# Kernel optimization log

Hardware: AMD Instinct MI355X
Metric: run time of the kernel (lower is better)

Reference implementation:

```python
import jax, jax.numpy as jnp
import numpy as np

D_MODEL = 1024
N_HEADS = 16
D_K = D_MODEL // N_HEADS  # 64


def setup_inputs() -> dict:
    key = jax.random.key(0)
    ks = jax.random.split(key, 12)
    B, S = 2, 2048
    inp = {
        "query": jax.random.normal(ks[0], (B, S, D_MODEL), jnp.float32),
        "key": jax.random.normal(ks[1], (B, S, D_MODEL), jnp.float32),
        "value": jax.random.normal(ks[2], (B, S, D_MODEL), jnp.float32),
        "mask": jnp.ones((B, 1, S, S), jnp.int32),
    }
    sc = 1.0 / np.sqrt(D_MODEL)
    inp["Wq"] = jax.random.normal(ks[3], (D_MODEL, D_MODEL), jnp.float32) * sc
    inp["bq"] = jnp.zeros((D_MODEL,), jnp.float32)
    inp["Wk"] = jax.random.normal(ks[4], (D_MODEL, D_MODEL), jnp.float32) * sc
    inp["bk"] = jnp.zeros((D_MODEL,), jnp.float32)
    inp["Wv"] = jax.random.normal(ks[5], (D_MODEL, D_MODEL), jnp.float32) * sc
    inp["bv"] = jnp.zeros((D_MODEL,), jnp.float32)
    inp["Wo"] = jax.random.normal(ks[6], (D_MODEL, D_MODEL), jnp.float32) * sc
    inp["bo"] = jnp.zeros((D_MODEL,), jnp.float32)
    return inp


def reference(query, key, value, mask, Wq, bq, Wk, bk, Wv, bv, Wo, bo):
    B, Sq, _ = query.shape
    H, dk = N_HEADS, D_K
    # linear projections, split heads: (B,S,D) -> (B,H,S,dk)
    def split_heads(x):
        return x.reshape(B, -1, H, dk).transpose(0, 2, 1, 3)
    Q = split_heads(query @ Wq.T + bq)
    K = split_heads(key @ Wk.T + bk)
    V = split_heads(value @ Wv.T + bv)
    scale = 1.0 / jnp.sqrt(jnp.asarray(dk, jnp.float32))
    scores = jnp.einsum('bhqd,bhkd->bhqk', Q, K) * scale
    scores = jnp.where(mask == 0, jnp.asarray(-1e9, scores.dtype), scores)
    attn = jax.nn.softmax(scores, axis=-1)  # (B,H,Sq,Sk)
    out = jnp.einsum('bhqk,bhkd->bhqd', attn, V)
    out = out.transpose(0, 2, 1, 3).reshape(B, Sq, D_MODEL)
    out = out @ Wo.T + bo
    return out, attn
```

## Files before the change

kernel.cpp:

```cpp
#include <hip/hip_runtime.h>
#include <cstdint>
#include <cstddef>

#define DEV __device__ __forceinline__

#define LGKM_BARRIER() asm volatile("s_waitcnt lgkmcnt(0)\n\ts_barrier" ::: "memory")

typedef float f32x4 __attribute__((ext_vector_type(4)));
typedef __bf16 bf16x8 __attribute__((ext_vector_type(8)));
typedef unsigned short u16x8 __attribute__((ext_vector_type(8)));

static constexpr int D = 1024, H = 16, DK = 64, S = 2048, B = 2;
static constexpr int M_TOT = B * S;
static constexpr size_t OUT0 = (size_t)M_TOT * D;

DEV unsigned short f2bf(float f) {
  unsigned x = __builtin_bit_cast(unsigned, f);
  unsigned r = (x + 0x7fffu + ((x >> 16) & 1u)) >> 16;
  return (unsigned short)r;
}

DEV float bf2f(unsigned short u) {
  return __builtin_bit_cast(float, (unsigned)u << 16);
}

DEV f32x4 mfma_bf16(bf16x8 a, bf16x8 b, f32x4 c) {
  return __builtin_amdgcn_mfma_f32_16x16x32_bf16(a, b, c, 0, 0, 0);
}

DEV bf16x8 bc(u16x8 u) { return __builtin_bit_cast(bf16x8, u); }

template <int MODE>
DEV void proj_body(unsigned short* As, unsigned short* Bs,
                   const unsigned short* A, const unsigned short* W,
                   const float* bias, void* dst) {
  constexpr int BM = 128, BK = 32, LDT = 40;
  const int tid = threadIdx.x;
  const int lane = tid & 63, wave = tid >> 6;
  const int wrow = wave >> 1, wcol = wave & 1;
  const int l15 = lane & 15, kg = lane >> 4;
  const int m0 = blockIdx.y * BM, n0 = blockIdx.x * BM;
  const int srow = tid >> 1, scb = (tid & 1) * 16;

  f32x4 acc[4][4] = {};

  for (int kt = 0; kt < D; kt += BK) {
    {
      const unsigned short* ap = A + (size_t)(m0 + srow) * D + kt + scb;
      *(u16x8*)&As[srow * LDT + scb] = *(const u16x8*)ap;
      *(u16x8*)&As[srow * LDT + scb + 8] = *(const u16x8*)(ap + 8);

      const unsigned short* wp = W + (size_t)(n0 + srow) * D + kt + scb;
      *(u16x8*)&Bs[srow * LDT + scb] = *(const u16x8*)wp;
      *(u16x8*)&Bs[srow * LDT + scb + 8] = *(const u16x8*)(wp + 8);
    }
    __syncthreads();

    bf16x8 a[4], b[4];
#pragma unroll
    for (int i = 0; i < 4; i++)
      a[i] = bc(*(const u16x8*)&As[(wrow * 64 + i * 16 + l15) * LDT + kg * 8]);
#pragma unroll
    for (int i = 0; i < 4; i++)
      b[i] = bc(*(const u16x8*)&Bs[(wcol * 64 + i * 16 + l15) * LDT + kg * 8]);
#pragma unroll
    for (int mi = 0; mi < 4; mi++)
#pragma unroll
      for (int ni = 0; ni < 4; ni++) acc[mi][ni] = mfma_bf16(a[mi], b[ni], acc[mi][ni]);
    __syncthreads();
  }

#pragma unroll
  for (int mi = 0; mi < 4; mi++) {
#pragma unroll
    for (int ni = 0; ni < 4; ni++) {
      const int n = n0 + wcol * 64 + ni * 16 + l15;
      const float bval = bias[n];
#pragma unroll
      for (int r = 0; r < 4; r++) {
        const int m = m0 + wrow * 64 + mi * 16 + kg * 4 + r;
        float v = acc[mi][ni][r] + bval;
        if constexpr (MODE == 0) v *= 0.125f;
        if constexpr (MODE == 0 || MODE == 1) {
          const int b_ = m >> 11, s = m & (S - 1), h = n >> 6, d_ = n & (DK - 1);
          ((unsigned short*)dst)[(((size_t)(b_ * H + h)) * S + s) * DK + d_] = f2bf(v);
        } else if constexpr (MODE == 2) {
          const int b_ = m >> 11, s = m & (S - 1), h = n >> 6, d_ = n & (DK - 1);
          ((unsigned short*)dst)[(((size_t)(b_ * H + h)) * DK + d_) * S + s] = f2bf(v);
        } else {
          ((float*)dst)[(size_t)m * D + n] = v;
        }
      }
    }
  }
}

struct ConvArgs {
  const float* src[7];
  unsigned short* dst[7];
  const int* mask;
  unsigned long long* bits;
};

__global__ __launch_bounds__(256) void conv_kernel(ConvArgs ca) {
  const int gid = blockIdx.x, tid = threadIdx.x;
  if (gid < 1024) {
    int seg, local;
    if (gid < 256) { seg = gid >> 6; local = gid & 63; }
    else { seg = 4 + ((gid - 256) >> 8); local = (gid - 256) & 255; }
    const float* src = ca.src[seg];
    unsigned short* dst = ca.dst[seg];
    const size_t off = (size_t)local * 16384;
#pragma unroll
    for (int it = 0; it < 4; it++) {
      const size_t i0 = off + it * 4096 + (size_t)tid * 16;
      float4 v0 = *(const float4*)(src + i0);
      float4 v1 = *(const float4*)(src + i0 + 4);
      float4 v2 = *(const float4*)(src + i0 + 8);
      float4 v3 = *(const float4*)(src + i0 + 12);
      u16x8 t0, t1;
      t0[0] = f2bf(v0.x); t0[1] = f2bf(v0.y); t0[2] = f2bf(v0.z); t0[3] = f2bf(v0.w);
      t0[4] = f2bf(v1.x); t0[5] = f2bf(v1.y); t0[6] = f2bf(v1.z); t0[7] = f2bf(v1.w);
      t1[0] = f2bf(v2.x); t1[1] = f2bf(v2.y); t1[2] = f2bf(v2.z); t1[3] = f2bf(v2.w);
      t1[4] = f2bf(v3.x); t1[5] = f2bf(v3.y); t1[6] = f2bf(v3.z); t1[7] = f2bf(v3.w);
      *(u16x8*)(dst + i0) = t0;
      *(u16x8*)(dst + i0 + 8) = t1;
    }
  } else {
    const int lane = tid & 63;
    const int base = (gid - 1024) * 256;
    for (int w = base + (tid >> 6); w < base + 256; w += 4) {
      int m = __builtin_nontemporal_load(ca.mask + (size_t)w * 64 + lane);
      unsigned long long bal = __ballot(m != 0);
      if (lane == 0) ca.bits[w] = bal;
    }
  }
}

struct GemmArgs {
  const unsigned short* Ab[3];
  const unsigned short* Wb[3];
  const float* bias[3];
  unsigned short* dst[3];
};

__global__ __launch_bounds__(256) void qkv_gemm(GemmArgs ga) {
  __shared__ __align__(16) unsigned short As[128 * 40];
  __shared__ __align__(16) unsigned short Bs[128 * 40];
  const int z = blockIdx.z;
  if (z == 0)
    proj_body<0>(As, Bs, ga.Ab[0], ga.Wb[0], ga.bias[0], ga.dst[0]);
  else if (z == 1)
    proj_body<1>(As, Bs, ga.Ab[1], ga.Wb[1], ga.bias[1], ga.dst[1]);
  else
    proj_body<2>(As, Bs, ga.Ab[2], ga.Wb[2], ga.bias[2], ga.dst[2]);
}

__global__ __launch_bounds__(256) void out_proj(const unsigned short* __restrict__ ctx,
                                                const unsigned short* __restrict__ Wob,
                                                const float* __restrict__ bo,
                                                float* __restrict__ out) {
  __shared__ __align__(16) unsigned short As[128 * 40];
  __shared__ __align__(16) unsigned short Bs[128 * 40];
  proj_body<3>(As, Bs, ctx, Wob, bo, out);
}

__global__ __launch_bounds__(512, 4) void attn_kernel(
    const unsigned short* __restrict__ Qb, const unsigned short* __restrict__ Kb,
    const unsigned short* __restrict__ Vt, const unsigned* __restrict__ bits32,
    float* __restrict__ attn_out, unsigned short* __restrict__ ctx) {
  constexpr int QB = 32;
  constexpr int PROW = 264;
  __shared__ __align__(16) unsigned short pbuf[2][QB * PROW];
  __shared__ float rsum[8 * QB];
  __shared__ float rinv_s[QB];
  __shared__ unsigned mflag;

  const int wg = blockIdx.x;
  const int qblk = wg & 63, h = (wg >> 6) & 15, b_ = wg >> 10;
  const int bh = b_ * H + h;
  const int qb0 = qblk * QB;
  const int tid = threadIdx.x, lane = tid & 63, wave = tid >> 6;
  const int l15 = lane & 15, kg = lane >> 4;
  const int rowq = kg * 4;
  constexpr float LOG2E = 1.44269504088896340736f;

  const unsigned* mrow = bits32 + ((size_t)b_ * S + qb0) * 64;

  if (tid == 0) mflag = 1u;
  __syncthreads();
  {
    unsigned ok = 1u;
#pragma unroll
    for (int i = 0; i < 4; i++)
      ok &= (mrow[tid + i * 512] == 0xFFFFFFFFu) ? 1u : 0u;
    if (!ok) atomicAnd(&mflag, 0u);
  }

  const unsigned short* qbase = Qb + ((size_t)bh * S + qb0) * DK;
  bf16x8 aq[2][2];
#pragma unroll
  for (int rg = 0; rg < 2; rg++)
#pragma unroll
    for (int hf = 0; hf < 2; hf++)
      aq[rg][hf] =
          bc(*(const u16x8*)(qbase + (size_t)(rg * 16 + l15) * DK + hf * 32 + kg * 8));
  __syncthreads();
  const bool allones = (mflag != 0u);

  float sum[2][4] = {};
#pragma unroll 2
  for (int i = 0; i < 16; i++) {
    const int t = wave * 16 + i;
    const unsigned short* krow = Kb + ((size_t)bh * S + t * 16 + l15) * DK;
    bf16x8 b0 = bc(*(const u16x8*)(krow + kg * 8));
    bf16x8 b1 = bc(*(const u16x8*)(krow + 32 + kg * 8));
    const unsigned shift = (unsigned)((t & 1) * 16 + l15);
#pragma unroll
    for (int rg = 0; rg < 2; rg++) {
      f32x4 c = {0.f, 0.f, 0.f, 0.f};
      c = mfma_bf16(aq[rg][0], b0, c);
      c = mfma_bf16(aq[rg][1], b1, c);
      if (allones) {
#pragma unroll
        for (int r = 0; r < 4; r++) sum[rg][r] += exp2f(c[r] * LOG2E);
      } else {
#pragma unroll
        for (int r = 0; r < 4; r++) {
          const unsigned w = mrow[(rg * 16 + rowq + r) * 64 + (t >> 1)];
          sum[rg][r] += ((w >> shift) & 1u) ? exp2f(c[r] * LOG2E) : 0.f;
        }
      }
    }
  }

#pragma unroll
  for (int rg = 0; rg < 2; rg++)
#pragma unroll
    for (int r = 0; r < 4; r++) {
      float s = sum[rg][r];
      s += __shfl_xor(s, 1);
      s += __shfl_xor(s, 2);
      s += __shfl_xor(s, 4);
      s += __shfl_xor(s, 8);
      if (l15 == 0) rsum[wave * QB + rg * 16 + rowq + r] = s;
    }
  __syncthreads();
  if (tid < QB) {
    float t2 = 0.f;
#pragma unroll
    for (int w = 0; w < 8; w++) t2 += rsum[w * QB + tid];
    rinv_s[tid] = 1.f / t2;
  }
  __syncthreads();

  float ri[2][4];
#pragma unroll
  for (int rg = 0; rg < 2; rg++)
#pragma unroll
    for (int r = 0; r < 4; r++) ri[rg][r] = rinv_s[rg * 16 + rowq + r];

  const int dg = wave & 3, ksub = wave >> 2;
  const unsigned short* vrow = Vt + ((size_t)bh * DK + dg * 16 + l15) * S + ksub * 128;
  float* abase = attn_out + ((size_t)bh * S + qb0) * S;
  const int wrow2 = lane >> 5;
  const int wcol = (lane & 31) * 8;
  f32x4 o[2] = {};

  auto writeDuty = [&](int sbw) {
    const unsigned short* pb = pbuf[sbw & 1];
#pragma unroll
    for (int rr = 0; rr < 2; rr++) {
      const int row = wave * 4 + rr * 2 + wrow2;
      u16x8 u = *(const u16x8*)&pb[row * PROW + wcol];
      f32x4 lo, hi;
      lo[0] = bf2f(u[0]); lo[1] = bf2f(u[1]); lo[2] = bf2f(u[2]); lo[3] = bf2f(u[3]);
      hi[0] = bf2f(u[4]); hi[1] = bf2f(u[5]); hi[2] = bf2f(u[6]); hi[3] = bf2f(u[7]);
      float* dp = abase + (size_t)row * S + sbw * 256 + wcol;
      __builtin_nontemporal_store(lo, (f32x4*)dp);
      __builtin_nontemporal_store(hi, (f32x4*)(dp + 4));
    }
  };

  for (int sb = 0; sb < 8; sb++) {
    if (sb) writeDuty(sb - 1);

    unsigned short* pb = pbuf[sb & 1];
#pragma unroll
    for (int j = 0; j < 2; j++) {
      const int t = sb * 16 + wave * 2 + j;
      const unsigned short* krow = Kb + ((size_t)bh * S + t * 16 + l15) * DK;
      bf16x8 b0 = bc(*(const u16x8*)(krow + kg * 8));
      bf16x8 b1 = bc(*(const u16x8*)(krow + 32 + kg * 8));
      const unsigned shift = (unsigned)((t & 1) * 16 + l15);
      const int lc = (wave * 2 + j) * 16 + l15;
#pragma unroll
      for (int rg = 0; rg < 2; rg++) {
        f32x4 c = {0.f, 0.f, 0.f, 0.f};
        c = mfma_bf16(aq[rg][0], b0, c);
        c = mfma_bf16(aq[rg][1], b1, c);
        if (allones) {
#pragma unroll
          for (int r = 0; r < 4; r++) {
            const int row = rg * 16 + rowq + r;
            pb[row * PROW + lc] = f2bf(exp2f(c[r] * LOG2E) * ri[rg][r]);
          }
        } else {
#pragma unroll
          for (int r = 0; r < 4; r++) {
            const int row = rg * 16 + rowq + r;
            const unsigned w = mrow[row * 64 + (t >> 1)];
            const float e = ((w >> shift) & 1u) ? exp2f(c[r] * LOG2E) : 0.f;
            pb[row * PROW + lc] = f2bf(e * ri[rg][r]);
          }
        }
      }
    }
    LGKM_BARRIER();

    const unsigned short* vv = vrow + sb * 256;
#pragma unroll
    for (int ks = 0; ks < 4; ks++) {
      bf16x8 bv = bc(*(const u16x8*)(vv + ks * 32 + kg * 8));
#pragma unroll
      for (int rg = 0; rg < 2; rg++) {
        bf16x8 af = bc(
            *(const u16x8*)&pb[(rg * 16 + l15) * PROW + ksub * 128 + ks * 32 + kg * 8]);
        o[rg] = mfma_bf16(af, bv, o[rg]);
      }
    }
  }
  writeDuty(7);

  float* opart = (float*)&pbuf[0][0];
  __syncthreads();
  if (ksub == 1) {
#pragma unroll
    for (int rg = 0; rg < 2; rg++)
#pragma unroll
      for (int r = 0; r < 4; r++)
        opart[dg * (QB * 17) + (rg * 16 + rowq + r) * 17 + l15] = o[rg][r];
  }
  __syncthreads();
  if (ksub == 0) {
#pragma unroll
    for (int rg = 0; rg < 2; rg++)
#pragma unroll
      for (int r = 0; r < 4; r++) {
        const int row = rg * 16 + rowq + r;
        const float v = o[rg][r] + opart[dg * (QB * 17) + row * 17 + l15];
        ctx[((size_t)(b_ * S + qb0 + row)) * D + h * DK + dg * 16 + l15] = f2bf(v);
      }
  }
}

extern "C" void kernel_launch(void* const* d_in, const int* in_sizes, int n_in,
                              void* d_out, int out_size, void* d_ws, size_t ws_size,
                              hipStream_t stream) {
  const float* query = (const float*)d_in[0];
  const float* key   = (const float*)d_in[1];
  const float* value = (const float*)d_in[2];
  const int*   mask  = (const int*)d_in[3];
  const float* Wq = (const float*)d_in[4];
  const float* bq = (const float*)d_in[5];
  const float* Wk = (const float*)d_in[6];
  const float* bk = (const float*)d_in[7];
  const float* Wv = (const float*)d_in[8];
  const float* bv = (const float*)d_in[9];
  const float* Wo = (const float*)d_in[10];
  const float* bo = (const float*)d_in[11];

  float* out_p = (float*)d_out;
  float* attn_p = (float*)d_out + OUT0;

  size_t off = 0;
  auto carve = [&](size_t bytes) {
    void* p = (char*)d_ws + off;
    off += (bytes + 255) & ~(size_t)255;
    return p;
  };
  const size_t headed = (size_t)B * H * S * DK * sizeof(unsigned short);
  const size_t wbytes = (size_t)D * D * sizeof(unsigned short);
  const size_t inbytes = (size_t)M_TOT * D * sizeof(unsigned short);
  unsigned short* Qb = (unsigned short*)carve(headed);
  unsigned short* Kb = (unsigned short*)carve(headed);
  unsigned short* Vt = (unsigned short*)carve(headed);
  unsigned short* ctx = (unsigned short*)carve(inbytes);
  unsigned long long* bits = (unsigned long long*)carve((size_t)B * S * S / 8);
  unsigned short* Wqb = (unsigned short*)carve(wbytes);
  unsigned short* Wkb = (unsigned short*)carve(wbytes);
  unsigned short* Wvb = (unsigned short*)carve(wbytes);
  unsigned short* Wob = (unsigned short*)carve(wbytes);
  unsigned short* Qin = (unsigned short*)carve(inbytes);
  unsigned short* Kin = (unsigned short*)carve(inbytes);
  unsigned short* Vin = (unsigned short*)carve(inbytes);

  ConvArgs ca;
  ca.src[0] = Wq; ca.src[1] = Wk; ca.src[2] = Wv; ca.src[3] = Wo;
  ca.src[4] = query; ca.src[5] = key; ca.src[6] = value;
  ca.dst[0] = Wqb; ca.dst[1] = Wkb; ca.dst[2] = Wvb; ca.dst[3] = Wob;
  ca.dst[4] = Qin; ca.dst[5] = Kin; ca.dst[6] = Vin;
  ca.mask = mask; ca.bits = bits;
  conv_kernel<<<1536, 256, 0, stream>>>(ca);

  GemmArgs ga;
  ga.Ab[0] = Qin; ga.Ab[1] = Kin; ga.Ab[2] = Vin;
  ga.Wb[0] = Wqb; ga.Wb[1] = Wkb; ga.Wb[2] = Wvb;
  ga.bias[0] = bq; ga.bias[1] = bk; ga.bias[2] = bv;
  ga.dst[0] = Qb; ga.dst[1] = Kb; ga.dst[2] = Vt;
  qkv_gemm<<<dim3(8, 32, 3), 256, 0, stream>>>(ga);

  attn_kernel<<<B * H * (S / 32), 512, 0, stream>>>(Qb, Kb, Vt, (const unsigned*)bits,
                                                    attn_p, ctx);

  out_proj<<<dim3(8, 32), 256, 0, stream>>>(ctx, Wob, bo, out_p);
}
```

Baseline: 378.6 us.

## Halve attention query tile and drop split-K reduction of context

The attention kernel now processes 16 query rows per block with 4 waves instead of 32 rows with 8 waves. Each wave owns one 16-wide slice of the head dimension over the full key range, so the cross-wave partial-sum reduction through shared memory and its two barriers go away. Launching twice as many smaller blocks is meant to improve occupancy and load balance. In exchange, K and V tiles are re-read by twice as many blocks, and each wave does more serial MFMA work.

Result: slower. 514.7 us (+35.9%).

```diff
diff --git a/kernel.cpp b/kernel.cpp
--- a/kernel.cpp
+++ b/kernel.cpp
@@ -165,19 +165,19 @@
   proj_body<3>(As, Bs, ctx, Wob, bo, out);
 }
 
-__global__ __launch_bounds__(512, 4) void attn_kernel(
+__global__ __launch_bounds__(256, 4) void attn_kernel(
     const unsigned short* __restrict__ Qb, const unsigned short* __restrict__ Kb,
     const unsigned short* __restrict__ Vt, const unsigned* __restrict__ bits32,
     float* __restrict__ attn_out, unsigned short* __restrict__ ctx) {
-  constexpr int QB = 32;
+  constexpr int QB = 16;
   constexpr int PROW = 264;
   __shared__ __align__(16) unsigned short pbuf[2][QB * PROW];
-  __shared__ float rsum[8 * QB];
+  __shared__ float rsum[4 * QB];
   __shared__ float rinv_s[QB];
   __shared__ unsigned mflag;
 
   const int wg = blockIdx.x;
-  const int qblk = wg & 63, h = (wg >> 6) & 15, b_ = wg >> 10;
+  const int qblk = wg & 127, h = (wg >> 7) & 15, b_ = wg >> 11;
   const int bh = b_ * H + h;
   const int qb0 = qblk * QB;
   const int tid = threadIdx.x, lane = tid & 63, wave = tid >> 6;
@@ -193,79 +193,67 @@
     unsigned ok = 1u;
 #pragma unroll
     for (int i = 0; i < 4; i++)
-      ok &= (mrow[tid + i * 512] == 0xFFFFFFFFu) ? 1u : 0u;
+      ok &= (mrow[tid + i * 256] == 0xFFFFFFFFu) ? 1u : 0u;
     if (!ok) atomicAnd(&mflag, 0u);
   }
 
   const unsigned short* qbase = Qb + ((size_t)bh * S + qb0) * DK;
-  bf16x8 aq[2][2];
-#pragma unroll
-  for (int rg = 0; rg < 2; rg++)
-#pragma unroll
-    for (int hf = 0; hf < 2; hf++)
-      aq[rg][hf] =
-          bc(*(const u16x8*)(qbase + (size_t)(rg * 16 + l15) * DK + hf * 32 + kg * 8));
+  bf16x8 aq0 = bc(*(const u16x8*)(qbase + (size_t)l15 * DK + kg * 8));
+  bf16x8 aq1 = bc(*(const u16x8*)(qbase + (size_t)l15 * DK + 32 + kg * 8));
   __syncthreads();
   const bool allones = (mflag != 0u);
 
-  float sum[2][4] = {};
+  float sum[4] = {0.f, 0.f, 0.f, 0.f};
 #pragma unroll 2
-  for (int i = 0; i < 16; i++) {
-    const int t = wave * 16 + i;
+  for (int i = 0; i < 32; i++) {
+    const int t = wave * 32 + i;
     const unsigned short* krow = Kb + ((size_t)bh * S + t * 16 + l15) * DK;
     bf16x8 b0 = bc(*(const u16x8*)(krow + kg * 8));
     bf16x8 b1 = bc(*(const u16x8*)(krow + 32 + kg * 8));
     const unsigned shift = (unsigned)((t & 1) * 16 + l15);
-#pragma unroll
-    for (int rg = 0; rg < 2; rg++) {
-      f32x4 c = {0.f, 0.f, 0.f, 0.f};
-      c = mfma_bf16(aq[rg][0], b0, c);
-      c = mfma_bf16(aq[rg][1], b1, c);
-      if (allones) {
-#pragma unroll
-        for (int r = 0; r < 4; r++) sum[rg][r] += exp2f(c[r] * LOG2E);
-      } else {
-#pragma unroll
-        for (int r = 0; r < 4; r++) {
-          const unsigned w = mrow[(rg * 16 + rowq + r) * 64 + (t >> 1)];
-          sum[rg][r] += ((w >> shift) & 1u) ? exp2f(c[r] * LOG2E) : 0.f;
-        }
+    f32x4 c = {0.f, 0.f, 0.f, 0.f};
+    c = mfma_bf16(aq0, b0, c);
+    c = mfma_bf16(aq1, b1, c);
+    if (allones) {
+#pragma unroll
+      for (int r = 0; r < 4; r++) sum[r] += exp2f(c[r] * LOG2E);
+    } else {
+#pragma unroll
+      for (int r = 0; r < 4; r++) {
+        const unsigned w = mrow[(rowq + r) * 64 + (t >> 1)];
+        sum[r] += ((w >> shift) & 1u) ? exp2f(c[r] * LOG2E) : 0.f;
       }
     }
   }
 
 #pragma unroll
-  for (int rg = 0; rg < 2; rg++)
-#pragma unroll
-    for (int r = 0; r < 4; r++) {
-      float s = sum[rg][r];
-      s += __shfl_xor(s, 1);
-      s += __shfl_xor(s, 2);
-      s += __shfl_xor(s, 4);
-      s += __shfl_xor(s, 8);
-      if (l15 == 0) rsum[wave * QB + rg * 16 + rowq + r] = s;
-    }
+  for (int r = 0; r < 4; r++) {
+    float s = sum[r];
+    s += __shfl_xor(s, 1);
+    s += __shfl_xor(s, 2);
+    s += __shfl_xor(s, 4);
+    s += __shfl_xor(s, 8);
+    if (l15 == 0) rsum[wave * QB + rowq + r] = s;
+  }
   __syncthreads();
   if (tid < QB) {
     float t2 = 0.f;
 #pragma unroll
-    for (int w = 0; w < 8; w++) t2 += rsum[w * QB + tid];
+    for (int w = 0; w < 4; w++) t2 += rsum[w * QB + tid];
     rinv_s[tid] = 1.f / t2;
   }
   __syncthreads();
 
-  float ri[2][4];
-#pragma unroll
-  for (int rg = 0; rg < 2; rg++)
-#pragma unroll
-    for (int r = 0; r < 4; r++) ri[rg][r] = rinv_s[rg * 16 + rowq + r];
-
-  const int dg = wave & 3, ksub = wave >> 2;
-  const unsigned short* vrow = Vt + ((size_t)bh * DK + dg * 16 + l15) * S + ksub * 128;
+  float ri[4];
+#pragma unroll
+  for (int r = 0; r < 4; r++) ri[r] = rinv_s[rowq + r];
+
+  const int dg = wave;
+  const unsigned short* vrow = Vt + ((size_t)bh * DK + dg * 16 + l15) * S;
   float* abase = attn_out + ((size_t)bh * S + qb0) * S;
   const int wrow2 = lane >> 5;
   const int wcol = (lane & 31) * 8;
-  f32x4 o[2] = {};
+  f32x4 o = {0.f, 0.f, 0.f, 0.f};
 
   auto writeDuty = [&](int sbw) {
     const unsigned short* pb = pbuf[sbw & 1];
@@ -287,32 +275,26 @@
 
     unsigned short* pb = pbuf[sb & 1];
 #pragma unroll
-    for (int j = 0; j < 2; j++) {
-      const int t = sb * 16 + wave * 2 + j;
+    for (int j = 0; j < 4; j++) {
+      const int t = sb * 16 + wave * 4 + j;
       const unsigned short* krow = Kb + ((size_t)bh * S + t * 16 + l15) * DK;
       bf16x8 b0 = bc(*(const u16x8*)(krow + kg * 8));
       bf16x8 b1 = bc(*(const u16x8*)(krow + 32 + kg * 8));
       const unsigned shift = (unsigned)((t & 1) * 16 + l15);
-      const int lc = (wave * 2 + j) * 16 + l15;
-#pragma unroll
-      for (int rg = 0; rg < 2; rg++) {
-        f32x4 c = {0.f, 0.f, 0.f, 0.f};
-        c = mfma_bf16(aq[rg][0], b0, c);
-        c = mfma_bf16(aq[rg][1], b1, c);
-        if (allones) {
-#pragma unroll
-          for (int r = 0; r < 4; r++) {
-            const int row = rg * 16 + rowq + r;
-            pb[row * PROW + lc] = f2bf(exp2f(c[r] * LOG2E) * ri[rg][r]);
-          }
-        } else {
-#pragma unroll
-          for (int r = 0; r < 4; r++) {
-            const int row = rg * 16 + rowq + r;
-            const unsigned w = mrow[row * 64 + (t >> 1)];
-            const float e = ((w >> shift) & 1u) ? exp2f(c[r] * LOG2E) : 0.f;
-            pb[row * PROW + lc] = f2bf(e * ri[rg][r]);
-          }
+      const int lc = (wave * 4 + j) * 16 + l15;
+      f32x4 c = {0.f, 0.f, 0.f, 0.f};
+      c = mfma_bf16(aq0, b0, c);
+      c = mfma_bf16(aq1, b1, c);
+      if (allones) {
+#pragma unroll
+        for (int r = 0; r < 4; r++)
+          pb[(rowq + r) * PROW + lc] = f2bf(exp2f(c[r] * LOG2E) * ri[r]);
+      } else {
+#pragma unroll
+        for (int r = 0; r < 4; r++) {
+          const unsigned w = mrow[(rowq + r) * 64 + (t >> 1)];
+          const float e = ((w >> shift) & 1u) ? exp2f(c[r] * LOG2E) : 0.f;
+          pb[(rowq + r) * PROW + lc] = f2bf(e * ri[r]);
         }
       }
     }
@@ -320,37 +302,18 @@
 
     const unsigned short* vv = vrow + sb * 256;
 #pragma unroll
-    for (int ks = 0; ks < 4; ks++) {
+    for (int ks = 0; ks < 8; ks++) {
       bf16x8 bv = bc(*(const u16x8*)(vv + ks * 32 + kg * 8));
-#pragma unroll
-      for (int rg = 0; rg < 2; rg++) {
-        bf16x8 af = bc(
-            *(const u16x8*)&pb[(rg * 16 + l15) * PROW + ksub * 128 + ks * 32 + kg * 8]);
-        o[rg] = mfma_bf16(af, bv, o[rg]);
-      }
+      bf16x8 af = bc(*(const u16x8*)&pb[l15 * PROW + ks * 32 + kg * 8]);
+      o = mfma_bf16(af, bv, o);
     }
   }
   writeDuty(7);
 
-  float* opart = (float*)&pbuf[0][0];
-  __syncthreads();
-  if (ksub == 1) {
-#pragma unroll
-    for (int rg = 0; rg < 2; rg++)
-#pragma unroll
-      for (int r = 0; r < 4; r++)
-        opart[dg * (QB * 17) + (rg * 16 + rowq + r) * 17 + l15] = o[rg][r];
-  }
-  __syncthreads();
-  if (ksub == 0) {
-#pragma unroll
-    for (int rg = 0; rg < 2; rg++)
-#pragma unroll
-      for (int r = 0; r < 4; r++) {
-        const int row = rg * 16 + rowq + r;
-        const float v = o[rg][r] + opart[dg * (QB * 17) + row * 17 + l15];
-        ctx[((size_t)(b_ * S + qb0 + row)) * D + h * DK + dg * 16 + l15] = f2bf(v);
-      }
+#pragma unroll
+  for (int r = 0; r < 4; r++) {
+    const int row = rowq + r;
+    ctx[((size_t)(b_ * S + qb0 + row)) * D + h * DK + dg * 16 + l15] = f2bf(o[r]);
   }
 }
 
@@ -410,7 +373,7 @@
   ga.dst[0] = Qb; ga.dst[1] = Kb; ga.dst[2] = Vt;
   qkv_gemm<<<dim3(8, 32, 3), 256, 0, stream>>>(ga);
 
-  attn_kernel<<<B * H * (S / 32), 512, 0, stream>>>(Qb, Kb, Vt, (const unsigned*)bits,
+  attn_kernel<<<B * H * (S / 16), 256, 0, stream>>>(Qb, Kb, Vt, (const unsigned*)bits,
                                                     attn_p, ctx);
 
   out_proj<<<dim3(8, 32), 256, 0, stream>>>(ctx, Wob, bo, out_p);
```
